# Kernel tuning notes

Measured on AMD Instinct MI355X. Metric: run time of the kernel, lower is better.

The kernel has to match this reference:

```python
import jax, jax.numpy as jnp
import numpy as np

TIME_LEN = 8
JOINT_NUM = 22
SEQ = TIME_LEN * JOINT_NUM  # 176
H_NUM = 8
H_DIM = 32
NEG_BIG = -9e15


def _temporal_mask():
    # ones everywhere, except block-diagonal joint x joint blocks zeroed, plus identity
    m = np.ones((SEQ, SEQ), dtype=np.float32)
    for i in range(TIME_LEN):
        m[i * JOINT_NUM:(i + 1) * JOINT_NUM, i * JOINT_NUM:(i + 1) * JOINT_NUM] = 0.0
    spatial = 1.0 - m
    temporal = m + np.eye(SEQ, dtype=np.float32)
    return jnp.asarray(temporal), jnp.asarray(spatial)


def setup_inputs() -> dict:
    key = jax.random.key(0)
    ks = jax.random.split(key, 4)
    B, S, D_in = 256, SEQ, 128
    D_model = H_NUM * H_DIM
    s = 1.0 / np.sqrt(D_in)
    return {
        "x": jax.random.normal(ks[0], (B, S, D_in), dtype=jnp.float32),
        "Wq": jax.random.normal(ks[1], (D_in, D_model), dtype=jnp.float32) * s,
        "bq": jnp.zeros((D_model,), dtype=jnp.float32),
        "Wk": jax.random.normal(ks[2], (D_in, D_model), dtype=jnp.float32) * s,
        "bk": jnp.zeros((D_model,), dtype=jnp.float32),
        "Wv": jax.random.normal(ks[3], (D_in, D_model), dtype=jnp.float32) * s,
        "bv": jnp.zeros((D_model,), dtype=jnp.float32),
    }


def reference(x, Wq, bq, Wk, bk, Wv, bv):
    B = x.shape[0]
    mask, _ = _temporal_mask()  # att_type == 'temporal'

    def split_heads(t):  # [B,S,H*D] -> [B,H,S,D]
        return t.reshape(B, SEQ, H_NUM, H_DIM).transpose(0, 2, 1, 3)

    q = split_heads(x @ Wq + bq)
    k = split_heads(x @ Wk + bk)
    v = split_heads(jax.nn.relu(x @ Wv + bv))  # value map has ReLU

    scores = jnp.einsum("bhsd,bhtd->bhst", q, k) / jnp.sqrt(jnp.float32(H_DIM))
    scores = scores * mask + (1.0 - mask) * NEG_BIG
    att = jax.nn.softmax(scores, axis=-1)
    out = jnp.einsum("bhst,bhtd->bhsd", att, v)
    return out.transpose(0, 2, 1, 3).reshape(B, SEQ, H_NUM * H_DIM)
```

## Files before the change

### kernel.cpp

```cpp
#include <hip/hip_runtime.h>


#define SEQ    176
#define HD     32
#define DIN    128
#define DMODEL 256

typedef unsigned short ushort_t;
typedef __attribute__((ext_vector_type(8))) short short8;
typedef __attribute__((ext_vector_type(4))) float float4v;
typedef __attribute__((ext_vector_type(4))) unsigned short ushort4v;

#define WS_WT 0u
#define WS_X  196608u

#define SMEM_TOTAL 40192
#define OFF_QS 13056
#define OFF_KS 20096
#define OFF_VT 33792
#define P_STRIDE 3072

__device__ __forceinline__ ushort_t f2bf(float f) {
    union { float f; unsigned int u; } c; c.f = f;
    unsigned int u = c.u;
    unsigned int rb = 0x7FFFu + ((u >> 16) & 1u);
    return (ushort_t)((u + rb) >> 16);
}

__global__ __launch_bounds__(256)
void k0_conv(const float* __restrict__ x,
             const float* __restrict__ Wq, const float* __restrict__ Wk,
             const float* __restrict__ Wv,
             ushort_t* __restrict__ WT, ushort_t* __restrict__ X16)
{
    int bid = blockIdx.x;
    if (bid < 5632) {
        int f4 = bid * 256 + threadIdx.x;
        float4 v = reinterpret_cast<const float4*>(x)[f4];
        ushort4v o;
        o.x = f2bf(v.x); o.y = f2bf(v.y); o.z = f2bf(v.z); o.w = f2bf(v.w);
        reinterpret_cast<ushort4v*>(X16)[f4] = o;
    } else {
        int idx = (bid - 5632) * 256 + threadIdx.x;
        int e = idx * 4;
        int mat = e >> 15, h = (e >> 12) & 7, n = (e >> 7) & 31, k = e & 127;
        const float* W = (mat == 0) ? Wq : ((mat == 1) ? Wk : Wv);
        ushort4v o;
        o.x = f2bf(W[(k + 0) * DMODEL + h * HD + n]);
        o.y = f2bf(W[(k + 1) * DMODEL + h * HD + n]);
        o.z = f2bf(W[(k + 2) * DMODEL + h * HD + n]);
        o.w = f2bf(W[(k + 3) * DMODEL + h * HD + n]);
        reinterpret_cast<ushort4v*>(WT)[idx] = o;
    }
}

__global__ __launch_bounds__(704, 6)
void k1_attn(const ushort_t* __restrict__ X16, const ushort_t* __restrict__ WT,
             const float* __restrict__ bq, const float* __restrict__ bk,
             const float* __restrict__ bv, float* __restrict__ out)
{
    __shared__ ushort_t smem[SMEM_TOTAL];
    ushort_t* WS = smem;
    ushort_t* QS = smem + OFF_QS;
    ushort_t* KS = smem + OFF_KS;
    ushort_t* VT = smem + OFF_VT;

    const int tid  = threadIdx.x;
    const int lane = tid & 63;
    const int w    = tid >> 6;
    const int c    = lane & 15;
    const int q    = lane >> 4;
    const int b    = blockIdx.x >> 3;
    const int h    = blockIdx.x & 7;

#pragma unroll
    for (int it = 0; it < 3; ++it) {
        int c8 = tid + it * 704;
        if (c8 < 1536) {
            int mat = c8 >> 9, rem = c8 & 511, n = rem >> 4, kc = rem & 15;
            short8 v = *reinterpret_cast<const short8*>(
                WT + (size_t)(((mat * 8 + h) * 32 + n) * 128 + kc * 8));
            *reinterpret_cast<short8*>(WS + (mat * 32 + n) * 136 + kc * 8) = v;
        }
    }
    if (tid < 512) {
        VT[(tid >> 4) * 200 + 176 + (tid & 15)] = 0;
    }
    __syncthreads();

    const ushort_t* xr = X16 + ((size_t)b * SEQ + w * 16 + c) * DIN;
    short8 afr[4];
#pragma unroll
    for (int kk = 0; kk < 4; ++kk)
        afr[kk] = *reinterpret_cast<const short8*>(xr + kk * 32 + q * 8);

    const float qscale = 0.17677669529663687f * 1.4426950408889634f;

#pragma unroll
    for (int jj = 0; jj < 6; ++jj) {
        const int mat = jj >> 1, nt = jj & 1;
        const ushort_t* wrow = WS + (mat * 32 + nt * 16 + c) * 136 + q * 8;
        float4v acc = {0.f, 0.f, 0.f, 0.f};
        if (mat == 2) {
#pragma unroll
            for (int kk = 0; kk < 4; ++kk) {
                short8 bf = *reinterpret_cast<const short8*>(wrow + kk * 32);
                acc = __builtin_amdgcn_mfma_f32_16x16x32_bf16(bf, afr[kk], acc, 0, 0, 0);
            }
        } else {
#pragma unroll
            for (int kk = 0; kk < 4; ++kk) {
                short8 bf = *reinterpret_cast<const short8*>(wrow + kk * 32);
                acc = __builtin_amdgcn_mfma_f32_16x16x32_bf16(afr[kk], bf, acc, 0, 0, 0);
            }
        }
        const float* bias = (mat == 0) ? bq : ((mat == 1) ? bk : bv);
        float bia = bias[h * HD + nt * 16 + c];
        if (mat == 2) {
#pragma unroll
            for (int r = 0; r < 4; ++r) {
                float v = acc[r] + bia;
                v = v > 0.f ? v : 0.f;
                VT[(nt * 16 + q * 4 + r) * 200 + w * 16 + c] = f2bf(v);
            }
        } else if (mat == 0) {
#pragma unroll
            for (int r = 0; r < 4; ++r)
                QS[(w * 16 + q * 4 + r) * 40 + nt * 16 + c] =
                    f2bf((acc[r] + bia) * qscale);
        } else {
#pragma unroll
            for (int r = 0; r < 4; ++r)
                KS[(w * 16 + q * 4 + r) * 40 + nt * 16 + c] = f2bf(acc[r] + bia);
        }
    }
    __syncthreads();

    short8 afrag = *reinterpret_cast<const short8*>(QS + (w * 16 + c) * 40 + q * 8);
    float4v sc[11];
#pragma unroll
    for (int n = 0; n < 11; ++n) {
        short8 bf = *reinterpret_cast<const short8*>(KS + (n * 16 + c) * 40 + q * 8);
        float4v z = {0.f, 0.f, 0.f, 0.f};
        sc[n] = __builtin_amdgcn_mfma_f32_16x16x32_bf16(afrag, bf, z, 0, 0, 0);
    }

    int cb[11];
#pragma unroll
    for (int n = 0; n < 11; ++n) cb[n] = (n * 16 + c) / 22;
#pragma unroll
    for (int r = 0; r < 4; ++r) {
        int rg = w * 16 + q * 4 + r;
        int rb = rg / 22;
#pragma unroll
        for (int n = 0; n < 11; ++n) {
            int cg = n * 16 + c;
            if (cb[n] == rb && cg != rg) sc[n][r] = -1e30f;
        }
    }

    float inv[4];
#pragma unroll
    for (int r = 0; r < 4; ++r) {
        float s = 0.f;
#pragma unroll
        for (int n = 0; n < 11; ++n) {
            float e = __builtin_amdgcn_exp2f(sc[n][r]);
            sc[n][r] = e;
            s += e;
        }
        s += __shfl_xor(s, 1, 64);
        s += __shfl_xor(s, 2, 64);
        s += __shfl_xor(s, 4, 64);
        s += __shfl_xor(s, 8, 64);
        inv[r] = 1.0f / s;
    }

    __syncthreads();

    ushort_t* psw = smem + w * P_STRIDE;
#pragma unroll
    for (int n = 0; n < 11; ++n)
#pragma unroll
        for (int r = 0; r < 4; ++r)
            psw[(q * 4 + r) * 192 + n * 16 + c] = f2bf(sc[n][r]);
#pragma unroll
    for (int it = 0; it < 4; ++it) {
        int idx = lane + it * 64;
        psw[(idx >> 4) * 192 + 176 + (idx & 15)] = 0;
    }

    float4v o0 = {0.f, 0.f, 0.f, 0.f}, o1 = {0.f, 0.f, 0.f, 0.f};
    const ushort_t* prow = psw + c * 192;
    const ushort_t* v0p  = VT + c * 200;
    const ushort_t* v1p  = VT + (16 + c) * 200;
#pragma unroll
    for (int kk = 0; kk < 6; ++kk) {
        short8 pa = *reinterpret_cast<const short8*>(prow + kk * 32 + q * 8);
        short8 v0 = *reinterpret_cast<const short8*>(v0p + kk * 32 + q * 8);
        short8 v1 = *reinterpret_cast<const short8*>(v1p + kk * 32 + q * 8);
        o0 = __builtin_amdgcn_mfma_f32_16x16x32_bf16(pa, v0, o0, 0, 0, 0);
        o1 = __builtin_amdgcn_mfma_f32_16x16x32_bf16(pa, v1, o1, 0, 0, 0);
    }

    float* ob = out + ((size_t)b * SEQ + w * 16) * DMODEL + h * HD;
#pragma unroll
    for (int r = 0; r < 4; ++r) {
        ob[(q * 4 + r) * DMODEL + c]      = o0[r] * inv[r];
        ob[(q * 4 + r) * DMODEL + 16 + c] = o1[r] * inv[r];
    }
}

extern "C" void kernel_launch(void* const* d_in, const int* in_sizes, int n_in,
                              void* d_out, int out_size, void* d_ws, size_t ws_size,
                              hipStream_t stream) {
    const float* x  = (const float*)d_in[0];
    const float* Wq = (const float*)d_in[1];
    const float* bq = (const float*)d_in[2];
    const float* Wk = (const float*)d_in[3];
    const float* bk = (const float*)d_in[4];
    const float* Wv = (const float*)d_in[5];
    const float* bv = (const float*)d_in[6];
    float* out = (float*)d_out;

    char* ws = (char*)d_ws;
    ushort_t* WT  = (ushort_t*)(ws + WS_WT);
    ushort_t* X16 = (ushort_t*)(ws + WS_X);

    k0_conv<<<dim3(5728), dim3(256), 0, stream>>>(x, Wq, Wk, Wv, WT, X16);
    k1_attn<<<dim3(2048), dim3(704), 0, stream>>>(X16, WT, bq, bk, bv, out);
}
```

Measured before the change: 142.3 us.

## Keep Q and probabilities in registers via transposed MFMA layouts

The Q projection is computed transposed so each lane holds its Q fragment directly, and scores are computed as K·Qᵀ so the exponentiated probabilities land in registers in the layout the PV MFMA needs. This removes the Q and P shared-memory round trips and one block barrier, and shrinks LDS from about 80KB to about 53KB. Output is written with float4 stores. The risks are the permuted k-ordering in the K/V fragment assembly and extra register pressure from holding the pf array.

```diff
diff --git a/kernel.cpp b/kernel.cpp
--- a/kernel.cpp
+++ b/kernel.cpp
@@ -8,21 +8,20 @@
 
 typedef unsigned short ushort_t;
 typedef __attribute__((ext_vector_type(8))) short short8;
+typedef __attribute__((ext_vector_type(4))) short short4v;
 typedef __attribute__((ext_vector_type(4))) float float4v;
 typedef __attribute__((ext_vector_type(4))) unsigned short ushort4v;
 
 #define WS_WT 0u
 #define WS_X  196608u
 
-#define SMEM_TOTAL 40192
-#define OFF_QS 13056
-#define OFF_KS 20096
-#define OFF_VT 33792
-#define P_STRIDE 3072
+#define SMEM_TOTAL 26496
+#define OFF_KS 13056
+#define OFF_VT 20096
 
 __device__ __forceinline__ ushort_t f2bf(float f) {
-    union { float f; unsigned int u; } c; c.f = f;
-    unsigned int u = c.u;
+    union { float f; unsigned int u; } cv; cv.f = f;
+    unsigned int u = cv.u;
     unsigned int rb = 0x7FFFu + ((u >> 16) & 1u);
     return (ushort_t)((u + rb) >> 16);
 }
@@ -61,7 +60,6 @@
 {
     __shared__ ushort_t smem[SMEM_TOTAL];
     ushort_t* WS = smem;
-    ushort_t* QS = smem + OFF_QS;
     ushort_t* KS = smem + OFF_KS;
     ushort_t* VT = smem + OFF_VT;
 
@@ -89,125 +87,105 @@
     __syncthreads();
 
     const ushort_t* xr = X16 + ((size_t)b * SEQ + w * 16 + c) * DIN;
-    short8 afr[4];
+    short8 xf[4];
 #pragma unroll
     for (int kk = 0; kk < 4; ++kk)
-        afr[kk] = *reinterpret_cast<const short8*>(xr + kk * 32 + q * 8);
+        xf[kk] = *reinterpret_cast<const short8*>(xr + kk * 32 + q * 8);
 
     const float qscale = 0.17677669529663687f * 1.4426950408889634f;
 
-#pragma unroll
-    for (int jj = 0; jj < 6; ++jj) {
-        const int mat = jj >> 1, nt = jj & 1;
-        const ushort_t* wrow = WS + (mat * 32 + nt * 16 + c) * 136 + q * 8;
+    short8 qf8;
+#pragma unroll
+    for (int nt = 0; nt < 2; ++nt) {
+        const ushort_t* wrow = WS + (nt * 16 + c) * 136 + q * 8;
         float4v acc = {0.f, 0.f, 0.f, 0.f};
-        if (mat == 2) {
-#pragma unroll
-            for (int kk = 0; kk < 4; ++kk) {
-                short8 bf = *reinterpret_cast<const short8*>(wrow + kk * 32);
-                acc = __builtin_amdgcn_mfma_f32_16x16x32_bf16(bf, afr[kk], acc, 0, 0, 0);
-            }
-        } else {
-#pragma unroll
-            for (int kk = 0; kk < 4; ++kk) {
-                short8 bf = *reinterpret_cast<const short8*>(wrow + kk * 32);
-                acc = __builtin_amdgcn_mfma_f32_16x16x32_bf16(afr[kk], bf, acc, 0, 0, 0);
-            }
-        }
-        const float* bias = (mat == 0) ? bq : ((mat == 1) ? bk : bv);
-        float bia = bias[h * HD + nt * 16 + c];
-        if (mat == 2) {
-#pragma unroll
-            for (int r = 0; r < 4; ++r) {
-                float v = acc[r] + bia;
-                v = v > 0.f ? v : 0.f;
-                VT[(nt * 16 + q * 4 + r) * 200 + w * 16 + c] = f2bf(v);
-            }
-        } else if (mat == 0) {
-#pragma unroll
-            for (int r = 0; r < 4; ++r)
-                QS[(w * 16 + q * 4 + r) * 40 + nt * 16 + c] =
-                    f2bf((acc[r] + bia) * qscale);
-        } else {
-#pragma unroll
-            for (int r = 0; r < 4; ++r)
-                KS[(w * 16 + q * 4 + r) * 40 + nt * 16 + c] = f2bf(acc[r] + bia);
+#pragma unroll
+        for (int kk = 0; kk < 4; ++kk) {
+            short8 wf = *reinterpret_cast<const short8*>(wrow + kk * 32);
+            acc = __builtin_amdgcn_mfma_f32_16x16x32_bf16(wf, xf[kk], acc, 0, 0, 0);
+        }
+        float4 bb = *reinterpret_cast<const float4*>(bq + h * HD + nt * 16 + q * 4);
+        qf8[nt * 4 + 0] = (short)f2bf((acc[0] + bb.x) * qscale);
+        qf8[nt * 4 + 1] = (short)f2bf((acc[1] + bb.y) * qscale);
+        qf8[nt * 4 + 2] = (short)f2bf((acc[2] + bb.z) * qscale);
+        qf8[nt * 4 + 3] = (short)f2bf((acc[3] + bb.w) * qscale);
+    }
+#pragma unroll
+    for (int nt = 0; nt < 2; ++nt) {
+        const ushort_t* wrow = WS + (32 + nt * 16 + c) * 136 + q * 8;
+        float4v acc = {0.f, 0.f, 0.f, 0.f};
+#pragma unroll
+        for (int kk = 0; kk < 4; ++kk) {
+            short8 wf = *reinterpret_cast<const short8*>(wrow + kk * 32);
+            acc = __builtin_amdgcn_mfma_f32_16x16x32_bf16(xf[kk], wf, acc, 0, 0, 0);
+        }
+        float bia = bk[h * HD + nt * 16 + c];
+#pragma unroll
+        for (int r = 0; r < 4; ++r)
+            KS[(w * 16 + q * 4 + r) * 40 + nt * 16 + c] = f2bf(acc[r] + bia);
+    }
+#pragma unroll
+    for (int nt = 0; nt < 2; ++nt) {
+        const ushort_t* wrow = WS + (64 + nt * 16 + c) * 136 + q * 8;
+        float4v acc = {0.f, 0.f, 0.f, 0.f};
+#pragma unroll
+        for (int kk = 0; kk < 4; ++kk) {
+            short8 wf = *reinterpret_cast<const short8*>(wrow + kk * 32);
+            acc = __builtin_amdgcn_mfma_f32_16x16x32_bf16(wf, xf[kk], acc, 0, 0, 0);
+        }
+        float4 bb = *reinterpret_cast<const float4*>(bv + h * HD + nt * 16 + q * 4);
+#pragma unroll
+        for (int r = 0; r < 4; ++r) {
+            float bias_r = (r == 0) ? bb.x : (r == 1) ? bb.y : (r == 2) ? bb.z : bb.w;
+            float v = acc[r] + bias_r;
+            v = v > 0.f ? v : 0.f;
+            VT[(nt * 16 + q * 4 + r) * 200 + w * 16 + c] = f2bf(v);
         }
     }
     __syncthreads();
 
-    short8 afrag = *reinterpret_cast<const short8*>(QS + (w * 16 + c) * 40 + q * 8);
-    float4v sc[11];
+    const int t_row = w * 16 + c;
+    const int lo = (t_row / 22) * 22;
+    float su = 0.f;
+    short8 pf[6];
+    pf[5] = (short8){0, 0, 0, 0, 0, 0, 0, 0};
 #pragma unroll
     for (int n = 0; n < 11; ++n) {
-        short8 bf = *reinterpret_cast<const short8*>(KS + (n * 16 + c) * 40 + q * 8);
-        float4v z = {0.f, 0.f, 0.f, 0.f};
-        sc[n] = __builtin_amdgcn_mfma_f32_16x16x32_bf16(afrag, bf, z, 0, 0, 0);
-    }
-
-    int cb[11];
-#pragma unroll
-    for (int n = 0; n < 11; ++n) cb[n] = (n * 16 + c) / 22;
-#pragma unroll
-    for (int r = 0; r < 4; ++r) {
-        int rg = w * 16 + q * 4 + r;
-        int rb = rg / 22;
-#pragma unroll
-        for (int n = 0; n < 11; ++n) {
-            int cg = n * 16 + c;
-            if (cb[n] == rb && cg != rg) sc[n][r] = -1e30f;
-        }
-    }
-
-    float inv[4];
-#pragma unroll
-    for (int r = 0; r < 4; ++r) {
-        float s = 0.f;
-#pragma unroll
-        for (int n = 0; n < 11; ++n) {
-            float e = __builtin_amdgcn_exp2f(sc[n][r]);
-            sc[n][r] = e;
-            s += e;
-        }
-        s += __shfl_xor(s, 1, 64);
-        s += __shfl_xor(s, 2, 64);
-        s += __shfl_xor(s, 4, 64);
-        s += __shfl_xor(s, 8, 64);
-        inv[r] = 1.0f / s;
-    }
-
-    __syncthreads();
-
-    ushort_t* psw = smem + w * P_STRIDE;
-#pragma unroll
-    for (int n = 0; n < 11; ++n)
-#pragma unroll
-        for (int r = 0; r < 4; ++r)
-            psw[(q * 4 + r) * 192 + n * 16 + c] = f2bf(sc[n][r]);
-#pragma unroll
-    for (int it = 0; it < 4; ++it) {
-        int idx = lane + it * 64;
-        psw[(idx >> 4) * 192 + 176 + (idx & 15)] = 0;
-    }
-
-    float4v o0 = {0.f, 0.f, 0.f, 0.f}, o1 = {0.f, 0.f, 0.f, 0.f};
-    const ushort_t* prow = psw + c * 192;
-    const ushort_t* v0p  = VT + c * 200;
-    const ushort_t* v1p  = VT + (16 + c) * 200;
-#pragma unroll
-    for (int kk = 0; kk < 6; ++kk) {
-        short8 pa = *reinterpret_cast<const short8*>(prow + kk * 32 + q * 8);
-        short8 v0 = *reinterpret_cast<const short8*>(v0p + kk * 32 + q * 8);
-        short8 v1 = *reinterpret_cast<const short8*>(v1p + kk * 32 + q * 8);
-        o0 = __builtin_amdgcn_mfma_f32_16x16x32_bf16(pa, v0, o0, 0, 0, 0);
-        o1 = __builtin_amdgcn_mfma_f32_16x16x32_bf16(pa, v1, o1, 0, 0, 0);
-    }
-
-    float* ob = out + ((size_t)b * SEQ + w * 16) * DMODEL + h * HD;
-#pragma unroll
-    for (int r = 0; r < 4; ++r) {
-        ob[(q * 4 + r) * DMODEL + c]      = o0[r] * inv[r];
-        ob[(q * 4 + r) * DMODEL + 16 + c] = o1[r] * inv[r];
+        const ushort_t* krow = KS + (n * 16 + c) * 40;
+        short4v ka = *reinterpret_cast<const short4v*>(krow + q * 4);
+        short4v kb = *reinterpret_cast<const short4v*>(krow + 16 + q * 4);
+        short8 kf = {ka.x, ka.y, ka.z, ka.w, kb.x, kb.y, kb.z, kb.w};
+        float4v s = {0.f, 0.f, 0.f, 0.f};
+        s = __builtin_amdgcn_mfma_f32_16x16x32_bf16(kf, qf8, s, 0, 0, 0);
+#pragma unroll
+        for (int r = 0; r < 4; ++r) {
+            int tp = n * 16 + q * 4 + r;
+            float sv = (((unsigned)(tp - lo) < 22u) && (tp != t_row)) ? -1e30f : s[r];
+            float e = __builtin_amdgcn_exp2f(sv);
+            su += e;
+            pf[n >> 1][(n & 1) * 4 + r] = (short)f2bf(e);
+        }
+    }
+    su += __shfl_xor(su, 16, 64);
+    su += __shfl_xor(su, 32, 64);
+    const float invs = 1.0f / su;
+
+    float* ob = out + ((size_t)b * SEQ + t_row) * DMODEL + h * HD;
+#pragma unroll
+    for (int mt = 0; mt < 2; ++mt) {
+        const ushort_t* vrow = VT + (mt * 16 + c) * 200;
+        float4v o = {0.f, 0.f, 0.f, 0.f};
+#pragma unroll
+        for (int g = 0; g < 6; ++g) {
+            short4v va = *reinterpret_cast<const short4v*>(vrow + (2 * g) * 16 + q * 4);
+            short4v vb = *reinterpret_cast<const short4v*>(vrow + (2 * g + 1) * 16 + q * 4);
+            short8 vf = {va.x, va.y, va.z, va.w, vb.x, vb.y, vb.z, vb.w};
+            o = __builtin_amdgcn_mfma_f32_16x16x32_bf16(vf, pf[g], o, 0, 0, 0);
+        }
+        float4 st;
+        st.x = o[0] * invs; st.y = o[1] * invs;
+        st.z = o[2] * invs; st.w = o[3] * invs;
+        *reinterpret_cast<float4*>(ob + mt * 16 + q * 4) = st;
     }
 }
 
```

Result: faster. 133.4 us (-6.2%).
